# Performance work log

Measured on AMD Instinct MI355X. Metric: run time of the kernel, lower is better.

Reference implementation:

```python
import jax, jax.numpy as jnp
import numpy as np

# Pangu-Weather EarthAttention3D, dim=192 branch
H = 6                 # heads
D = 192               # dim
DH = D // H           # head dim = 32
N = 2 * 6 * 12        # window tokens = 144
TW = (8 // 2) * (186 // 6)  # type_of_windows = 124
NW = 8                # number of windows (leading batch axis)
SCALE = DH ** -0.5


def setup_inputs() -> dict:
    key = jax.random.key(0)
    ks = jax.random.split(key, 7)
    return {
        "x": jax.random.normal(ks[0], (NW, TW, N, D), jnp.float32),
        "mask": jax.random.normal(ks[1], (NW, TW, N, N), jnp.float32),
        "w_qkv": jax.random.normal(ks[2], (D, 3 * D), jnp.float32) * 0.02,
        "b_qkv": jnp.zeros((3 * D,), jnp.float32),
        "bias": jax.random.normal(ks[3], (1, TW, H, N, N), jnp.float32) * 0.02,
        "w_out": jax.random.normal(ks[4], (D, D), jnp.float32) * 0.02,
        "b_out": jnp.zeros((D,), jnp.float32),
    }


def reference(x, mask, w_qkv, b_qkv, bias, w_out, b_out):
    B, W, Ntok, Dm = x.shape  # (nW, type_of_windows, win_tokens, dim)
    # fused QKV projection
    qkv = (x @ w_qkv + b_qkv).reshape(B, W, Ntok, 3, H, DH)
    qkv = jnp.transpose(qkv, (3, 0, 1, 4, 2, 5))  # (3, B, W, H, N, dh)
    q, k, v = qkv[0] * SCALE, qkv[1], qkv[2]
    # scores + earth-specific bias + window mask (broadcast over heads)
    attn = jnp.einsum('bwhnd,bwhmd->bwhnm', q, k)
    attn = attn + bias + mask[:, :, None, :, :]
    attn = jax.nn.softmax(attn, axis=-1)  # dropout_rate=0 -> identity
    out = jnp.einsum('bwhnm,bwhmd->bwhnd', attn, v)
    out = jnp.transpose(out, (0, 1, 3, 2, 4)).reshape(B, W, Ntok, Dm)
    return out @ w_out + b_out
```

## Files before the change

### kernel.cpp

```cpp
#include <hip/hip_runtime.h>
#include <hip/hip_bf16.h>

typedef __bf16 bf16_t;
typedef bf16_t bf16x8 __attribute__((ext_vector_type(8)));
typedef bf16_t bf16x4 __attribute__((ext_vector_type(4)));
typedef float f32x4 __attribute__((ext_vector_type(4)));

#define SCALE 0.17677669529663687f

#define PIN(x) asm volatile("" : "+v"(x))

__device__ __forceinline__ int swz_elem(int r, int c) {
    int g = c >> 3;
    return r * 192 + ((g >> 3) << 6) + (((g & 7) ^ (r & 7)) << 3) + (c & 7);
}

__device__ __forceinline__ void stage_chunk(bf16_t* dst, const bf16_t* src, int tid) {
#pragma unroll
    for (int it = 0; it < 3; ++it) {
        int off = (it * 256 + tid) * 8;
        __builtin_amdgcn_global_load_lds(
            (const __attribute__((address_space(1))) unsigned int*)(src + off),
            (__attribute__((address_space(3))) unsigned int*)(dst + off),
            16, 0, 0);
    }
}

__global__ void prep_weights(const float* __restrict__ w_qkv, const float* __restrict__ w_out,
                             bf16_t* __restrict__ wqkvS, bf16_t* __restrict__ woutS) {
    int i = blockIdx.x * 256 + threadIdx.x;
    if (i < 576 * 192) {
        int o = i / 192, k = i % 192;
        float v = w_qkv[k * 576 + o];
        if (o < 192) v *= SCALE;
        wqkvS[(o >> 5) * 6144 + swz_elem(o & 31, k)] = (bf16_t)v;
    }
    if (i < 192 * 192) {
        int o = i / 192, k = i % 192;
        woutS[(o >> 5) * 6144 + swz_elem(o & 31, k)] = (bf16_t)w_out[k * 192 + o];
    }
}

__global__ __launch_bounds__(256, 4)
void qkv_gemm(const float* __restrict__ x, const float* __restrict__ b_qkv,
              const bf16_t* __restrict__ wqkvS,
              bf16_t* __restrict__ Qg, bf16_t* __restrict__ Kg, bf16_t* __restrict__ Vg)
{
    __shared__ __align__(16) bf16_t Wb[2][6144];
    __shared__ __align__(16) bf16_t T[4][2][16 * 40];
    const int tid  = threadIdx.x;
    const int lane = tid & 63;
    const int wave = tid >> 6;
    const int lrow = lane & 15;
    const int lgrp = lane >> 4;
    const int r0   = blockIdx.x * 128 + wave * 32;

    stage_chunk(&Wb[0][0], wqkvS, tid);

    bf16x8 af[2][6];
#pragma unroll
    for (int tt = 0; tt < 2; ++tt)
#pragma unroll
        for (int ks = 0; ks < 6; ++ks) {
            const float* px = x + (size_t)(r0 + tt * 16 + lrow) * 192 + ks * 32 + lgrp * 8;
            f32x4 lo = *(const f32x4*)px;
            f32x4 hi = *(const f32x4*)(px + 4);
            bf16x8 v;
            v[0] = (bf16_t)lo[0]; v[1] = (bf16_t)lo[1]; v[2] = (bf16_t)lo[2]; v[3] = (bf16_t)lo[3];
            v[4] = (bf16_t)hi[0]; v[5] = (bf16_t)hi[1]; v[6] = (bf16_t)hi[2]; v[7] = (bf16_t)hi[3];
            af[tt][ks] = v;
        }
    __syncthreads();

    for (int hc = 0; hc < 18; ++hc) {
        if (hc < 17) stage_chunk(&Wb[(hc + 1) & 1][0], wqkvS + (hc + 1) * 6144, tid);
        const bf16_t* wb = &Wb[hc & 1][0];

        f32x4 a[2][2];
        a[0][0] = f32x4{0.f,0.f,0.f,0.f}; a[0][1] = f32x4{0.f,0.f,0.f,0.f};
        a[1][0] = f32x4{0.f,0.f,0.f,0.f}; a[1][1] = f32x4{0.f,0.f,0.f,0.f};
#pragma unroll
        for (int ks = 0; ks < 6; ++ks) {
            bf16x8 wf0 = *(const bf16x8*)&wb[swz_elem(lrow,      ks * 32 + lgrp * 8)];
            bf16x8 wf1 = *(const bf16x8*)&wb[swz_elem(16 + lrow, ks * 32 + lgrp * 8)];
#pragma unroll
            for (int tt = 0; tt < 2; ++tt) {
                a[tt][0] = __builtin_amdgcn_mfma_f32_16x16x32_bf16(af[tt][ks], wf0, a[tt][0], 0, 0, 0);
                a[tt][1] = __builtin_amdgcn_mfma_f32_16x16x32_bf16(af[tt][ks], wf1, a[tt][1], 0, 0, 0);
            }
        }
        __syncthreads();

        float b0 = b_qkv[hc * 32 + lrow], b1 = b_qkv[hc * 32 + 16 + lrow];
        if (hc < 6) { b0 *= SCALE; b1 *= SCALE; }
        const int h = (hc < 6) ? hc : (hc < 12) ? hc - 6 : hc - 12;
        bf16_t* dst = (hc < 6) ? Qg : (hc < 12) ? Kg : Vg;
#pragma unroll
        for (int tt = 0; tt < 2; ++tt) {
#pragma unroll
            for (int j = 0; j < 4; ++j) {
                T[wave][tt][(lgrp * 4 + j) * 40 + lrow]      = (bf16_t)(a[tt][0][j] + b0);
                T[wave][tt][(lgrp * 4 + j) * 40 + 16 + lrow] = (bf16_t)(a[tt][1][j] + b1);
            }
            bf16x8 val = *(const bf16x8*)&T[wave][tt][lrow * 40 + lgrp * 8];
            int tk = r0 + tt * 16 + lrow, bw = tk / 144, n = tk % 144;
            *(bf16x8*)&dst[((size_t)(bw * 6 + h) * 144 + n) * 32 + lgrp * 8] = val;
        }
    }
}

__global__ __launch_bounds__(256, 4)
void vt_transpose(const bf16_t* __restrict__ Vg, bf16_t* __restrict__ Vt)
{
    __shared__ bf16_t tile[4][32 * 168];
    const int lane = threadIdx.x & 63;
    const int wave = threadIdx.x >> 6;
    const int gid  = blockIdx.x * 4 + wave;
    bf16_t* tl = &tile[wave][0];
    const bf16_t* src = Vg + (size_t)gid * 4608;
    bf16_t* dst = Vt + (size_t)gid * 5120;

#pragma unroll
    for (int it = 0; it < 9; ++it) {
        int u = it * 64 + lane;
        int row = u >> 2, dc = u & 3;
        bf16x8 v = *(const bf16x8*)(src + row * 32 + dc * 8);
#pragma unroll
        for (int i = 0; i < 8; ++i) tl[(dc * 8 + i) * 168 + row] = v[i];
    }
    {
        int d = lane >> 1, c = lane & 1;
        bf16x8 z = {};
        *(bf16x8*)&tl[d * 168 + 144 + c * 8] = z;
    }
#pragma unroll
    for (int it = 0; it < 10; ++it) {
        int u = it * 64 + lane;
        int d = u / 20, c = u % 20;
        *(bf16x8*)(dst + d * 160 + c * 8) = *(const bf16x8*)&tl[d * 168 + c * 8];
    }
}

__global__ __launch_bounds__(256, 4)
void earth_attn_v5(const bf16_t* __restrict__ Qg, const bf16_t* __restrict__ Kg,
                   const bf16_t* __restrict__ Vt,
                   const float* __restrict__ mask, const float* __restrict__ bias,
                   bf16_t* __restrict__ Og)
{
    __shared__ bf16_t P[4][16 * 168];
    const int tid  = threadIdx.x;
    const int lane = tid & 63;
    const int wave = tid >> 6;
    const int lrow = lane & 15;
    const int lgrp = lane >> 4;

    const int orig = blockIdx.x;
    const int blk  = (orig & 7) * 1674 + (orig >> 3);

    const int wid = blk * 4 + wave;
    const int ww  = wid / 432;
    const int r1  = wid - ww * 432;
    const int b   = r1 / 54;
    const int rem = r1 - b * 54;
    const int h   = rem / 9;
    const int t0  = (rem % 9) * 16;
    const int bw  = b * 124 + ww;

    const size_t kbase = ((size_t)(bw * 6 + h) * 144) * 32;
    const size_t vbase = ((size_t)(bw * 6 + h) * 32) * 160;

    bf16x8 qa = *(const bf16x8*)&Qg[kbase + (size_t)(t0 + lrow) * 32 + lgrp * 8];
    bf16x8 ka[9];
#pragma unroll
    for (int nt = 0; nt < 9; ++nt)
        ka[nt] = *(const bf16x8*)&Kg[kbase + (size_t)(nt * 16 + lrow) * 32 + lgrp * 8];
    PIN(qa);
#pragma unroll
    for (int nt = 0; nt < 9; ++nt) PIN(ka[nt]);

    bf16x8 va0[5], va1[5];
#pragma unroll
    for (int ks = 0; ks < 5; ++ks) {
        va0[ks] = *(const bf16x8*)&Vt[vbase + (size_t)lrow * 160 + ks * 32 + lgrp * 8];
        va1[ks] = *(const bf16x8*)&Vt[vbase + (size_t)(16 + lrow) * 160 + ks * 32 + lgrp * 8];
    }
#pragma unroll
    for (int ks = 0; ks < 5; ++ks) { PIN(va0[ks]); PIN(va1[ks]); }

    const float* bp = bias + ((size_t)(ww * 6 + h) * 144 + (t0 + lrow)) * 144;
    const float* mp = mask + ((size_t)bw * 144 + (t0 + lrow)) * 144;
    f32x4 s[9];
#pragma unroll
    for (int g = 0; g < 3; ++g) {
        f32x4 bv[3], mv[3];
#pragma unroll
        for (int i = 0; i < 3; ++i) {
            int nt = g * 3 + i;
            bv[i] = *(const f32x4*)(bp + nt * 16 + lgrp * 4);
            mv[i] = *(const f32x4*)(mp + nt * 16 + lgrp * 4);
        }
#pragma unroll
        for (int i = 0; i < 3; ++i) { PIN(bv[i]); PIN(mv[i]); }
#pragma unroll
        for (int i = 0; i < 3; ++i) {
            int nt = g * 3 + i;
            s[nt] = bv[i] + mv[i];
            s[nt] = __builtin_amdgcn_mfma_f32_16x16x32_bf16(ka[nt], qa, s[nt], 0, 0, 0);
        }
    }

    float mx = -1e30f;
#pragma unroll
    for (int nt = 0; nt < 9; ++nt)
#pragma unroll
        for (int j = 0; j < 4; ++j) mx = fmaxf(mx, s[nt][j]);
    mx = fmaxf(mx, __shfl_xor(mx, 16, 64));
    mx = fmaxf(mx, __shfl_xor(mx, 32, 64));
    float sum = 0.f;
#pragma unroll
    for (int nt = 0; nt < 9; ++nt)
#pragma unroll
        for (int j = 0; j < 4; ++j) { float e = __expf(s[nt][j] - mx); s[nt][j] = e; sum += e; }
    sum += __shfl_xor(sum, 16, 64);
    sum += __shfl_xor(sum, 32, 64);
    const float rinv = 1.0f / sum;

    bf16_t* pb = &P[wave][0];
#pragma unroll
    for (int nt = 0; nt < 9; ++nt) {
        bf16x4 pw;
#pragma unroll
        for (int j = 0; j < 4; ++j) pw[j] = (bf16_t)(s[nt][j] * rinv);
        *(bf16x4*)&pb[lrow * 168 + nt * 16 + lgrp * 4] = pw;
    }
    {
        uint2 z2 = make_uint2(0u, 0u);
        *(uint2*)&pb[lrow * 168 + 144 + lgrp * 4] = z2;
    }

    bf16x8 pa[5];
#pragma unroll
    for (int ks = 0; ks < 5; ++ks)
        pa[ks] = *(const bf16x8*)&pb[lrow * 168 + ks * 32 + lgrp * 8];
#pragma unroll
    for (int ks = 0; ks < 5; ++ks) PIN(pa[ks]);

    f32x4 o0{0.f, 0.f, 0.f, 0.f}, o1{0.f, 0.f, 0.f, 0.f};
#pragma unroll
    for (int ks = 0; ks < 5; ++ks) {
        o0 = __builtin_amdgcn_mfma_f32_16x16x32_bf16(pa[ks], va0[ks], o0, 0, 0, 0);
        o1 = __builtin_amdgcn_mfma_f32_16x16x32_bf16(pa[ks], va1[ks], o1, 0, 0, 0);
    }

#pragma unroll
    for (int j = 0; j < 4; ++j) {
        pb[(lgrp * 4 + j) * 168 + lrow]      = (bf16_t)o0[j];
        pb[(lgrp * 4 + j) * 168 + 16 + lrow] = (bf16_t)o1[j];
    }
    bf16x8 ov = *(const bf16x8*)&pb[lrow * 168 + lgrp * 8];
    *(bf16x8*)&Og[((size_t)bw * 144 + t0 + lrow) * 192 + h * 32 + lgrp * 8] = ov;
}

__global__ __launch_bounds__(256, 4)
void out_proj(const bf16_t* __restrict__ Og, const bf16_t* __restrict__ woutS,
              const float* __restrict__ b_out, float* __restrict__ out)
{
    __shared__ __align__(16) bf16_t Wb[2][6144];
    const int tid  = threadIdx.x;
    const int lane = tid & 63;
    const int wave = tid >> 6;
    const int lrow = lane & 15;
    const int lgrp = lane >> 4;
    const size_t row0 = (size_t)blockIdx.x * 64 + wave * 16;

    stage_chunk(&Wb[0][0], woutS, tid);

    bf16x8 af[6];
#pragma unroll
    for (int ks = 0; ks < 6; ++ks)
        af[ks] = *(const bf16x8*)(Og + (row0 + lrow) * 192 + ks * 32 + lgrp * 8);
    __syncthreads();

#pragma unroll
    for (int c = 0; c < 6; ++c) {
        if (c < 5) stage_chunk(&Wb[(c + 1) & 1][0], woutS + (c + 1) * 6144, tid);
        const bf16_t* wb = &Wb[c & 1][0];
        float b0 = b_out[c * 32 + lrow], b1 = b_out[c * 32 + 16 + lrow];
        f32x4 a0{b0, b0, b0, b0}, a1{b1, b1, b1, b1};
#pragma unroll
        for (int ks = 0; ks < 6; ++ks) {
            bf16x8 wf0 = *(const bf16x8*)&wb[swz_elem(lrow,      ks * 32 + lgrp * 8)];
            bf16x8 wf1 = *(const bf16x8*)&wb[swz_elem(16 + lrow, ks * 32 + lgrp * 8)];
            a0 = __builtin_amdgcn_mfma_f32_16x16x32_bf16(af[ks], wf0, a0, 0, 0, 0);
            a1 = __builtin_amdgcn_mfma_f32_16x16x32_bf16(af[ks], wf1, a1, 0, 0, 0);
        }
        __syncthreads();
#pragma unroll
        for (int j = 0; j < 4; ++j) {
            out[(row0 + lgrp * 4 + j) * 192 + c * 32 + lrow]      = a0[j];
            out[(row0 + lgrp * 4 + j) * 192 + c * 32 + 16 + lrow] = a1[j];
        }
    }
}

extern "C" void kernel_launch(void* const* d_in, const int* in_sizes, int n_in,
                              void* d_out, int out_size, void* d_ws, size_t ws_size,
                              hipStream_t stream) {
    const float* x     = (const float*)d_in[0];
    const float* mask  = (const float*)d_in[1];
    const float* w_qkv = (const float*)d_in[2];
    const float* b_qkv = (const float*)d_in[3];
    const float* bias  = (const float*)d_in[4];
    const float* w_out = (const float*)d_in[5];
    const float* b_out = (const float*)d_in[6];

    bf16_t* wqkvS = (bf16_t*)d_ws;
    bf16_t* woutS = wqkvS + 576 * 192;
    bf16_t* Qg    = woutS + 192 * 192;
    bf16_t* Kg    = Qg + (size_t)992 * 6 * 144 * 32;
    bf16_t* Vt    = Kg + (size_t)992 * 6 * 144 * 32;
    bf16_t* Og    = Vt + (size_t)992 * 6 * 32 * 160;
    bf16_t* Vg    = Og;

    prep_weights<<<dim3(432), dim3(256), 0, stream>>>(w_qkv, w_out, wqkvS, woutS);
    qkv_gemm<<<dim3(1116), dim3(256), 0, stream>>>(x, b_qkv, wqkvS, Qg, Kg, Vg);
    vt_transpose<<<dim3(1488), dim3(256), 0, stream>>>(Vg, Vt);
    earth_attn_v5<<<dim3(13392), dim3(256), 0, stream>>>(Qg, Kg, Vt, mask, bias, Og);
    out_proj<<<dim3(2232), dim3(256), 0, stream>>>(Og, woutS, b_out, (float*)d_out);
}
```

Baseline: 311.0 us.

## Loop each wave over all query tiles to reuse K/V registers

```diff
diff --git a/kernel.cpp b/kernel.cpp
--- a/kernel.cpp
+++ b/kernel.cpp
@@ -141,8 +141,8 @@
     }
 }
 
-__global__ __launch_bounds__(256, 4)
-void earth_attn_v5(const bf16_t* __restrict__ Qg, const bf16_t* __restrict__ Kg,
+__global__ __launch_bounds__(256, 2)
+void earth_attn_v6(const bf16_t* __restrict__ Qg, const bf16_t* __restrict__ Kg,
                    const bf16_t* __restrict__ Vt,
                    const float* __restrict__ mask, const float* __restrict__ bias,
                    bf16_t* __restrict__ Og)
@@ -155,28 +155,22 @@
     const int lgrp = lane >> 4;
 
     const int orig = blockIdx.x;
-    const int blk  = (orig & 7) * 1674 + (orig >> 3);
+    const int blk  = (orig & 7) * 186 + (orig >> 3);
 
     const int wid = blk * 4 + wave;
-    const int ww  = wid / 432;
-    const int r1  = wid - ww * 432;
-    const int b   = r1 / 54;
-    const int rem = r1 - b * 54;
-    const int h   = rem / 9;
-    const int t0  = (rem % 9) * 16;
+    const int ww  = wid / 48;
+    const int r1  = wid % 48;
+    const int b   = r1 / 6;
+    const int h   = r1 % 6;
     const int bw  = b * 124 + ww;
 
     const size_t kbase = ((size_t)(bw * 6 + h) * 144) * 32;
     const size_t vbase = ((size_t)(bw * 6 + h) * 32) * 160;
 
-    bf16x8 qa = *(const bf16x8*)&Qg[kbase + (size_t)(t0 + lrow) * 32 + lgrp * 8];
     bf16x8 ka[9];
 #pragma unroll
     for (int nt = 0; nt < 9; ++nt)
         ka[nt] = *(const bf16x8*)&Kg[kbase + (size_t)(nt * 16 + lrow) * 32 + lgrp * 8];
-    PIN(qa);
-#pragma unroll
-    for (int nt = 0; nt < 9; ++nt) PIN(ka[nt]);
 
     bf16x8 va0[5], va1[5];
 #pragma unroll
@@ -184,81 +178,93 @@
         va0[ks] = *(const bf16x8*)&Vt[vbase + (size_t)lrow * 160 + ks * 32 + lgrp * 8];
         va1[ks] = *(const bf16x8*)&Vt[vbase + (size_t)(16 + lrow) * 160 + ks * 32 + lgrp * 8];
     }
-#pragma unroll
-    for (int ks = 0; ks < 5; ++ks) { PIN(va0[ks]); PIN(va1[ks]); }
-
-    const float* bp = bias + ((size_t)(ww * 6 + h) * 144 + (t0 + lrow)) * 144;
-    const float* mp = mask + ((size_t)bw * 144 + (t0 + lrow)) * 144;
-    f32x4 s[9];
-#pragma unroll
-    for (int g = 0; g < 3; ++g) {
-        f32x4 bv[3], mv[3];
-#pragma unroll
-        for (int i = 0; i < 3; ++i) {
-            int nt = g * 3 + i;
-            bv[i] = *(const f32x4*)(bp + nt * 16 + lgrp * 4);
-            mv[i] = *(const f32x4*)(mp + nt * 16 + lgrp * 4);
-        }
-#pragma unroll
-        for (int i = 0; i < 3; ++i) { PIN(bv[i]); PIN(mv[i]); }
-#pragma unroll
-        for (int i = 0; i < 3; ++i) {
-            int nt = g * 3 + i;
-            s[nt] = bv[i] + mv[i];
-            s[nt] = __builtin_amdgcn_mfma_f32_16x16x32_bf16(ka[nt], qa, s[nt], 0, 0, 0);
-        }
-    }
-
-    float mx = -1e30f;
-#pragma unroll
-    for (int nt = 0; nt < 9; ++nt)
-#pragma unroll
-        for (int j = 0; j < 4; ++j) mx = fmaxf(mx, s[nt][j]);
-    mx = fmaxf(mx, __shfl_xor(mx, 16, 64));
-    mx = fmaxf(mx, __shfl_xor(mx, 32, 64));
-    float sum = 0.f;
-#pragma unroll
-    for (int nt = 0; nt < 9; ++nt)
-#pragma unroll
-        for (int j = 0; j < 4; ++j) { float e = __expf(s[nt][j] - mx); s[nt][j] = e; sum += e; }
-    sum += __shfl_xor(sum, 16, 64);
-    sum += __shfl_xor(sum, 32, 64);
-    const float rinv = 1.0f / sum;
-
+
+    const float* bp_base = bias + (size_t)(ww * 6 + h) * 144 * 144;
+    const float* mp_base = mask + (size_t)bw * 144 * 144;
     bf16_t* pb = &P[wave][0];
-#pragma unroll
-    for (int nt = 0; nt < 9; ++nt) {
-        bf16x4 pw;
-#pragma unroll
-        for (int j = 0; j < 4; ++j) pw[j] = (bf16_t)(s[nt][j] * rinv);
-        *(bf16x4*)&pb[lrow * 168 + nt * 16 + lgrp * 4] = pw;
-    }
-    {
-        uint2 z2 = make_uint2(0u, 0u);
-        *(uint2*)&pb[lrow * 168 + 144 + lgrp * 4] = z2;
-    }
-
-    bf16x8 pa[5];
-#pragma unroll
-    for (int ks = 0; ks < 5; ++ks)
-        pa[ks] = *(const bf16x8*)&pb[lrow * 168 + ks * 32 + lgrp * 8];
-#pragma unroll
-    for (int ks = 0; ks < 5; ++ks) PIN(pa[ks]);
-
-    f32x4 o0{0.f, 0.f, 0.f, 0.f}, o1{0.f, 0.f, 0.f, 0.f};
-#pragma unroll
-    for (int ks = 0; ks < 5; ++ks) {
-        o0 = __builtin_amdgcn_mfma_f32_16x16x32_bf16(pa[ks], va0[ks], o0, 0, 0, 0);
-        o1 = __builtin_amdgcn_mfma_f32_16x16x32_bf16(pa[ks], va1[ks], o1, 0, 0, 0);
-    }
-
-#pragma unroll
-    for (int j = 0; j < 4; ++j) {
-        pb[(lgrp * 4 + j) * 168 + lrow]      = (bf16_t)o0[j];
-        pb[(lgrp * 4 + j) * 168 + 16 + lrow] = (bf16_t)o1[j];
-    }
-    bf16x8 ov = *(const bf16x8*)&pb[lrow * 168 + lgrp * 8];
-    *(bf16x8*)&Og[((size_t)bw * 144 + t0 + lrow) * 192 + h * 32 + lgrp * 8] = ov;
+    bf16_t* ogp = Og + ((size_t)bw * 144) * 192 + h * 32 + lgrp * 8;
+
+    bf16x8 qa = *(const bf16x8*)&Qg[kbase + (size_t)lrow * 32 + lgrp * 8];
+
+#pragma unroll 1
+    for (int t = 0; t < 9; ++t) {
+        const int tn = (t < 8) ? t + 1 : 8;
+        bf16x8 qa_n = *(const bf16x8*)&Qg[kbase + (size_t)(tn * 16 + lrow) * 32 + lgrp * 8];
+
+        const float* bp = bp_base + (size_t)(t * 16 + lrow) * 144;
+        const float* mp = mp_base + (size_t)(t * 16 + lrow) * 144;
+        f32x4 s[9];
+#pragma unroll
+        for (int g = 0; g < 3; ++g) {
+            f32x4 bv[3], mv[3];
+#pragma unroll
+            for (int i = 0; i < 3; ++i) {
+                int nt = g * 3 + i;
+                bv[i] = *(const f32x4*)(bp + nt * 16 + lgrp * 4);
+                mv[i] = *(const f32x4*)(mp + nt * 16 + lgrp * 4);
+            }
+#pragma unroll
+            for (int i = 0; i < 3; ++i) { PIN(bv[i]); PIN(mv[i]); }
+#pragma unroll
+            for (int i = 0; i < 3; ++i) {
+                int nt = g * 3 + i;
+                s[nt] = bv[i] + mv[i];
+                s[nt] = __builtin_amdgcn_mfma_f32_16x16x32_bf16(ka[nt], qa, s[nt], 0, 0, 0);
+            }
+        }
+
+        float mx = -1e30f;
+#pragma unroll
+        for (int nt = 0; nt < 9; ++nt)
+#pragma unroll
+            for (int j = 0; j < 4; ++j) mx = fmaxf(mx, s[nt][j]);
+        mx = fmaxf(mx, __shfl_xor(mx, 16, 64));
+        mx = fmaxf(mx, __shfl_xor(mx, 32, 64));
+        float sum = 0.f;
+#pragma unroll
+        for (int nt = 0; nt < 9; ++nt)
+#pragma unroll
+            for (int j = 0; j < 4; ++j) { float e = __expf(s[nt][j] - mx); s[nt][j] = e; sum += e; }
+        sum += __shfl_xor(sum, 16, 64);
+        sum += __shfl_xor(sum, 32, 64);
+        const float rinv = 1.0f / sum;
+
+#pragma unroll
+        for (int nt = 0; nt < 9; ++nt) {
+            bf16x4 pw;
+#pragma unroll
+            for (int j = 0; j < 4; ++j) pw[j] = (bf16_t)(s[nt][j] * rinv);
+            *(bf16x4*)&pb[lrow * 168 + nt * 16 + lgrp * 4] = pw;
+        }
+        {
+            uint2 z2 = make_uint2(0u, 0u);
+            *(uint2*)&pb[lrow * 168 + 144 + lgrp * 4] = z2;
+        }
+
+        bf16x8 pa[5];
+#pragma unroll
+        for (int ks = 0; ks < 5; ++ks)
+            pa[ks] = *(const bf16x8*)&pb[lrow * 168 + ks * 32 + lgrp * 8];
+#pragma unroll
+        for (int ks = 0; ks < 5; ++ks) PIN(pa[ks]);
+
+        f32x4 o0{0.f, 0.f, 0.f, 0.f}, o1{0.f, 0.f, 0.f, 0.f};
+#pragma unroll
+        for (int ks = 0; ks < 5; ++ks) {
+            o0 = __builtin_amdgcn_mfma_f32_16x16x32_bf16(pa[ks], va0[ks], o0, 0, 0, 0);
+            o1 = __builtin_amdgcn_mfma_f32_16x16x32_bf16(pa[ks], va1[ks], o1, 0, 0, 0);
+        }
+
+#pragma unroll
+        for (int j = 0; j < 4; ++j) {
+            pb[(lgrp * 4 + j) * 168 + lrow]      = (bf16_t)o0[j];
+            pb[(lgrp * 4 + j) * 168 + 16 + lrow] = (bf16_t)o1[j];
+        }
+        bf16x8 ov = *(const bf16x8*)&pb[lrow * 168 + lgrp * 8];
+        *(bf16x8*)(ogp + (size_t)(t * 16 + lrow) * 192) = ov;
+
+        qa = qa_n;
+    }
 }
 
 __global__ __launch_bounds__(256, 4)
@@ -325,6 +331,6 @@
     prep_weights<<<dim3(432), dim3(256), 0, stream>>>(w_qkv, w_out, wqkvS, woutS);
     qkv_gemm<<<dim3(1116), dim3(256), 0, stream>>>(x, b_qkv, wqkvS, Qg, Kg, Vg);
     vt_transpose<<<dim3(1488), dim3(256), 0, stream>>>(Vg, Vt);
-    earth_attn_v5<<<dim3(13392), dim3(256), 0, stream>>>(Qg, Kg, Vt, mask, bias, Og);
+    earth_attn_v6<<<dim3(1488), dim3(256), 0, stream>>>(Qg, Kg, Vt, mask, bias, Og);
     out_proj<<<dim3(2232), dim3(256), 0, stream>>>(Og, woutS, b_out, (float*)d_out);
 }
```

Measured after the change: 269.9 us. -13.2%, faster.
